# Performance work log

Hardware: AMD Instinct MI355X
Metric: run time of the kernel (lower is better)

## Reference

```python
import jax, jax.numpy as jnp
import numpy as np

N_CELL, N_WELL = 200000, 2000
E_CC, E_CW = 1200000, 200000
CF, WF, H = 16, 8, 128
NUM_PHASES, OUT_SEQ = 3, 25
OUT = NUM_PHASES * OUT_SEQ  # 75


def setup_inputs() -> dict:
    key = jax.random.key(0)
    ks = jax.random.split(key, 24)
    p = lambda k, shp: jax.random.normal(k, shp, dtype=jnp.float32) * 0.02
    return {
        "cell_x": jax.random.normal(ks[0], (N_CELL, CF), dtype=jnp.float32),
        "well_x": jax.random.normal(ks[1], (N_WELL, WF), dtype=jnp.float32),
        "edge_index_cell": jax.random.randint(ks[2], (2, E_CC), 0, N_CELL),
        "edge_well_src": jax.random.randint(ks[3], (E_CW,), 0, N_CELL),
        "edge_well_dst": jax.random.randint(ks[4], (E_CW,), 0, N_WELL),
        # input projections
        "W_cell": p(ks[5], (CF, H)), "b_cell": jnp.zeros((H,), jnp.float32),
        "W_well": p(ks[6], (WF, H)), "b_well": jnp.zeros((H,), jnp.float32),
        # SAGEConv cell->cell: lin_l (on aggregated neighbors, has bias), lin_r (on root, no bias)
        "Wl_cc": p(ks[7], (H, H)), "bl_cc": jnp.zeros((H,), jnp.float32),
        "Wr_cc": p(ks[8], (H, H)),
        # SAGEConv cell->well (bipartite)
        "Wl_cw": p(ks[9], (H, H)), "bl_cw": jnp.zeros((H,), jnp.float32),
        "Wr_cw": p(ks[10], (H, H)),
        # well MLP
        "W_m1": p(ks[11], (H, H)), "b_m1": jnp.zeros((H,), jnp.float32),
        "W_m2": p(ks[12], (H, OUT)), "b_m2": jnp.zeros((OUT,), jnp.float32),
    }


def _mean_aggr(msgs, dst, num_segments):
    # PyG 'mean' aggregation: sum per destination / neighbor count; 0 for isolated nodes.
    s = jax.ops.segment_sum(msgs, dst, num_segments=num_segments)
    c = jax.ops.segment_sum(jnp.ones((dst.shape[0], 1), msgs.dtype), dst, num_segments=num_segments)
    return s / jnp.maximum(c, 1.0)


def reference(cell_x, well_x, edge_index_cell, edge_well_src, edge_well_dst,
              W_cell, b_cell, W_well, b_well,
              Wl_cc, bl_cc, Wr_cc, Wl_cw, bl_cw, Wr_cw,
              W_m1, b_m1, W_m2, b_m2):
    cell_h = cell_x @ W_cell + b_cell                      # [N_cell, H]
    well_h = well_x @ W_well + b_well                      # [N_well, H]

    # SAGEConv(cell_h, edge_index_cell): gather source feats, mean-scatter to dst
    src, dst = edge_index_cell[0], edge_index_cell[1]
    agg_c = _mean_aggr(cell_h[src], dst, N_CELL)           # [N_cell, H]
    cell_h = agg_c @ Wl_cc + bl_cc + cell_h @ Wr_cc

    # Bipartite SAGEConv((cell_h, well_h), edge_well): aggregate cells into wells
    agg_w = _mean_aggr(cell_h[edge_well_src], edge_well_dst, N_WELL)  # [N_well, H]
    well_h = agg_w @ Wl_cw + bl_cw + well_h @ Wr_cw

    # well MLP head
    h = jax.nn.relu(well_h @ W_m1 + b_m1)
    out = h @ W_m2 + b_m2                                  # [N_well, 75]
    return out.reshape(-1, NUM_PHASES, OUT_SEQ)            # [N_well, 3, 25]
```

## Files before the change

### kernel.cpp

```cpp
#include <hip/hip_runtime.h>

#define N_CELL 200000
#define N_WELL 2000
#define E_CC   1200000
#define E_CW   200000
#define CF     16
#define WF     8
#define H      128
#define OUTF   75

#define CAP_C  16
#define CAP_W  224
#define OVF_CAP 16384
#define WPB    4

#define BLD_T  307200

__device__ __forceinline__ float b2f(unsigned short u) {
    union { unsigned int i; float f; } v; v.i = ((unsigned int)u) << 16; return v.f;
}
__device__ __forceinline__ unsigned short f2b(float f) {
    union { float f; unsigned int i; } v; v.f = f;
    unsigned int i = v.i;
    return (unsigned short)((i + 0x7fffu + ((i >> 16) & 1u)) >> 16);
}
__device__ __forceinline__ float lo16(unsigned int v) { return b2f((unsigned short)(v & 0xffffu)); }
__device__ __forceinline__ float hi16(unsigned int v) { return b2f((unsigned short)(v >> 16)); }
__device__ __forceinline__ float ldf(const void* p, int i, int bf) {
    return bf ? b2f(((const unsigned short*)p)[i]) : ((const float*)p)[i];
}

__device__ __forceinline__ int sniff128(const unsigned int* __restrict__ x)
{
    __shared__ int cnt[128];
    int t = threadIdx.x;
    unsigned a = x[t], b = x[t + 128];
    unsigned ea = (a >> 7) & 0xffu, eb = (b >> 7) & 0xffu;
    cnt[t] = ((ea >= 110u && ea <= 135u) ? 1 : 0) + ((eb >= 110u && eb <= 135u) ? 1 : 0);
    __syncthreads();
    for (int o = 64; o > 0; o >>= 1) { if (t < o) cnt[t] += cnt[t + o]; __syncthreads(); }
    int r = (cnt[0] >= 192) ? 1 : 0;
    __syncthreads();
    return r;
}

__global__ __launch_bounds__(128) void k_setup1(const unsigned int* __restrict__ x256,
                                                const void* __restrict__ W_cell,
                                                const void* __restrict__ b_cell,
                                                const void* __restrict__ Wl,
                                                const void* __restrict__ Wr,
                                                const void* __restrict__ bl,
                                                float* __restrict__ G1, float* __restrict__ G2,
                                                float* __restrict__ g1v, float* __restrict__ g2v,
                                                int* __restrict__ flag,
                                                unsigned int* __restrict__ zero_p, int zero_dw)
{
    int f = threadIdx.x, b = blockIdx.x;
    if (b < 16) {
        int bf = sniff128(x256);
        float s1 = 0.f, s2 = 0.f;
        for (int j = 0; j < H; ++j) {
            float wc = ldf(W_cell, b * H + j, bf);
            s1 += wc * ldf(Wl, j * H + f, bf);
            s2 += wc * ldf(Wr, j * H + f, bf);
        }
        G1[b * H + f] = s1; G2[b * H + f] = s2;
    } else if (b == 16) {
        int bf = sniff128(x256);
        float s1 = 0.f, s2 = 0.f;
        for (int j = 0; j < H; ++j) {
            float bc = ldf(b_cell, j, bf);
            s1 += bc * ldf(Wl, j * H + f, bf);
            s2 += bc * ldf(Wr, j * H + f, bf);
        }
        g1v[f] = s1; g2v[f] = s2 + ldf(bl, f, bf);
    } else if (b == 17) {
        int bf = sniff128(x256);
        if (f == 0) flag[0] = bf;
    } else {
        for (int i = (b - 18) * 128 + f; i < zero_dw; i += 64 * 128)
            zero_p[i] = 0u;
    }
}

__global__ __launch_bounds__(128) void k_setup2(const float* __restrict__ G1, const float* __restrict__ G2,
                                                const float* __restrict__ g1v, const float* __restrict__ g2v,
                                                const void* __restrict__ Wl_cw,
                                                const void* __restrict__ bl_cw,
                                                const void* __restrict__ Wr_cw,
                                                const void* __restrict__ W_well,
                                                const void* __restrict__ b_well,
                                                const void* __restrict__ Wm1, const void* __restrict__ Wm2,
                                                const void* __restrict__ bm1, const void* __restrict__ bm2,
                                                const int* __restrict__ flag,
                                                float* __restrict__ A1, float* __restrict__ A2,
                                                float* __restrict__ Bm,
                                                float* __restrict__ a1, float* __restrict__ a2,
                                                float* __restrict__ b0,
                                                float* __restrict__ Wm1f, float* __restrict__ Wm2f,
                                                float* __restrict__ bm1f, float* __restrict__ bm2f)
{
    int f = threadIdx.x, b = blockIdx.x, bf = flag[0];
    if (b < 16) {
        float s1 = 0.f, s2 = 0.f;
        for (int j = 0; j < H; ++j) {
            float wl = ldf(Wl_cw, j * H + f, bf);
            s1 += G1[b * H + j] * wl;
            s2 += G2[b * H + j] * wl;
        }
        A1[b * H + f] = s1; A2[b * H + f] = s2;
    } else if (b < 24) {
        int k = b - 16;
        float s = 0.f;
        for (int j = 0; j < H; ++j)
            s += ldf(W_well, k * H + j, bf) * ldf(Wr_cw, j * H + f, bf);
        Bm[k * H + f] = s;
    } else if (b == 24) {
        float s1 = 0.f, s2 = 0.f, s3 = 0.f;
        for (int j = 0; j < H; ++j) {
            float wl = ldf(Wl_cw, j * H + f, bf);
            s1 += g1v[j] * wl;
            s2 += g2v[j] * wl;
            s3 += ldf(b_well, j, bf) * ldf(Wr_cw, j * H + f, bf);
        }
        a1[f] = s1; a2[f] = s2; b0[f] = s3 + ldf(bl_cw, f, bf);
    } else {
        int i = (b - 25) * 128 + f;
        if (i < H * H) Wm1f[i] = ldf(Wm1, i, bf);
        else if (i < H * H + H * OUTF) Wm2f[i - H * H] = ldf(Wm2, i - H * H, bf);
        else if (i < H * H + H * OUTF + H) bm1f[i - H * H - H * OUTF] = ldf(bm1, i - H * H - H * OUTF, bf);
        else if (i < H * H + H * OUTF + H + OUTF) bm2f[i - H * H - H * OUTF - H] = ldf(bm2, i - H * H - H * OUTF - H, bf);
    }
}

__global__ void k_markw(const int* __restrict__ ews, const int* __restrict__ ewd,
                        unsigned char* __restrict__ mark,
                        int* __restrict__ counts_w, int* __restrict__ buckets_w)
{
    int i = blockIdx.x * 256 + threadIdx.x;
    if (i < E_CW) {
        unsigned c = (unsigned)ews[i];
        if (c < N_CELL) mark[c] = 1;
        unsigned d = (unsigned)ewd[i];
        if (d < N_WELL) {
            int s = atomicAdd(&counts_w[d], 1);
            if (s < CAP_W) buckets_w[d * CAP_W + s] = ews[i];
        }
    }
}

__global__ __launch_bounds__(256) void k_build(const int* __restrict__ cc_src, const int* __restrict__ cc_dst,
                                               const unsigned char* __restrict__ mark,
                                               int* __restrict__ counts_c,
                                               int* __restrict__ buckets_c,
                                               int* __restrict__ ovf_cnt, int2* __restrict__ ovf)
{
    int i = blockIdx.x * 256 + threadIdx.x;
    int e0 = i, e1 = i + BLD_T, e2 = i + 2 * BLD_T, e3 = i + 3 * BLD_T;
    unsigned d0 = (e0 < E_CC) ? (unsigned)cc_dst[e0] : 0xFFFFFFFFu;
    unsigned d1 = (e1 < E_CC) ? (unsigned)cc_dst[e1] : 0xFFFFFFFFu;
    unsigned d2 = (e2 < E_CC) ? (unsigned)cc_dst[e2] : 0xFFFFFFFFu;
    unsigned d3 = (e3 < E_CC) ? (unsigned)cc_dst[e3] : 0xFFFFFFFFu;
    bool m0 = (d0 < N_CELL) && mark[d0];
    bool m1 = (d1 < N_CELL) && mark[d1];
    bool m2 = (d2 < N_CELL) && mark[d2];
    bool m3 = (d3 < N_CELL) && mark[d3];
    int s0 = m0 ? cc_src[e0] : 0;
    int s1 = m1 ? cc_src[e1] : 0;
    int s2 = m2 ? cc_src[e2] : 0;
    int s3 = m3 ? cc_src[e3] : 0;
    if (m0) {
        int p = atomicAdd(&counts_c[d0], 1);
        if (p < CAP_C) buckets_c[d0 * CAP_C + p] = s0;
        else { int q = atomicAdd(ovf_cnt, 1); if (q < OVF_CAP) { ovf[q].x = (int)d0; ovf[q].y = s0; } }
    }
    if (m1) {
        int p = atomicAdd(&counts_c[d1], 1);
        if (p < CAP_C) buckets_c[d1 * CAP_C + p] = s1;
        else { int q = atomicAdd(ovf_cnt, 1); if (q < OVF_CAP) { ovf[q].x = (int)d1; ovf[q].y = s1; } }
    }
    if (m2) {
        int p = atomicAdd(&counts_c[d2], 1);
        if (p < CAP_C) buckets_c[d2 * CAP_C + p] = s2;
        else { int q = atomicAdd(ovf_cnt, 1); if (q < OVF_CAP) { ovf[q].x = (int)d2; ovf[q].y = s2; } }
    }
    if (m3) {
        int p = atomicAdd(&counts_c[d3], 1);
        if (p < CAP_C) buckets_c[d3 * CAP_C + p] = s3;
        else { int q = atomicAdd(ovf_cnt, 1); if (q < OVF_CAP) { ovf[q].x = (int)d3; ovf[q].y = s3; } }
    }
}

__global__ __launch_bounds__(256) void k_aggA(const void* __restrict__ xr,
                                              const int* __restrict__ flag,
                                              const unsigned char* __restrict__ mark,
                                              const int* __restrict__ counts_c,
                                              const int* __restrict__ buckets_c,
                                              float* __restrict__ y)
{
    int gid = (blockIdx.x * 256 + threadIdx.x) >> 3;
    int jl = threadIdx.x & 7;
    if (gid >= N_CELL) return;
    if (!mark[gid]) return;
    int bf = flag[0];
    int cnt = counts_c[gid]; if (cnt < 0) cnt = 0;
    int lim = (cnt < CAP_C) ? cnt : CAP_C;
    float acc[16];
#pragma unroll
    for (int k = 0; k < 16; ++k) acc[k] = 0.f;

    for (int j = jl; j < lim; j += 8) {
        unsigned s = (unsigned)buckets_c[gid * CAP_C + j]; if (s >= N_CELL) s = 0;
        if (bf) {
            uint4 a = ((const uint4*)xr)[(size_t)s * 2];
            uint4 b = ((const uint4*)xr)[(size_t)s * 2 + 1];
            acc[0] += lo16(a.x);  acc[1] += hi16(a.x);
            acc[2] += lo16(a.y);  acc[3] += hi16(a.y);
            acc[4] += lo16(a.z);  acc[5] += hi16(a.z);
            acc[6] += lo16(a.w);  acc[7] += hi16(a.w);
            acc[8] += lo16(b.x);  acc[9] += hi16(b.x);
            acc[10] += lo16(b.y); acc[11] += hi16(b.y);
            acc[12] += lo16(b.z); acc[13] += hi16(b.z);
            acc[14] += lo16(b.w); acc[15] += hi16(b.w);
        } else {
            const float4* p = (const float4*)xr + (size_t)s * 4;
#pragma unroll
            for (int q = 0; q < 4; ++q) {
                float4 v = p[q];
                acc[4 * q]     += v.x; acc[4 * q + 1] += v.y;
                acc[4 * q + 2] += v.z; acc[4 * q + 3] += v.w;
            }
        }
    }
#pragma unroll
    for (int m = 1; m < 8; m <<= 1) {
#pragma unroll
        for (int k = 0; k < 16; ++k) acc[k] += __shfl_xor(acc[k], m, 64);
    }
    float sc = (cnt > 0) ? (1.0f / (float)cnt) : 0.0f;
    float2 st; st.x = acc[2 * jl] * sc; st.y = acc[2 * jl + 1] * sc;
    ((float2*)y)[(size_t)gid * 8 + jl] = st;
}

__global__ __launch_bounds__(256) void k_ovf(const void* __restrict__ xr,
                                             const int* __restrict__ flag,
                                             const int* __restrict__ ovf_cnt,
                                             const int2* __restrict__ ovf,
                                             const int* __restrict__ counts_c,
                                             float* __restrict__ y)
{
    int gid = (blockIdx.x * 256 + threadIdx.x) >> 3;
    int jl = threadIdx.x & 7;
    int n = ovf_cnt[0]; if (n > OVF_CAP) n = OVF_CAP;
    if (gid >= n) return;
    int bf = flag[0];
    unsigned d = (unsigned)ovf[gid].x; if (d >= N_CELL) d = 0;
    unsigned s = (unsigned)ovf[gid].y; if (s >= N_CELL) s = 0;
    int cnt = counts_c[d];
    float inv = (cnt > 0) ? (1.0f / (float)cnt) : 0.0f;
    float v0, v1;
    if (bf) {
        unsigned int u = ((const unsigned int*)xr)[(size_t)s * 8 + jl];
        v0 = lo16(u); v1 = hi16(u);
    } else {
        v0 = ((const float*)xr)[(size_t)s * 16 + 2 * jl];
        v1 = ((const float*)xr)[(size_t)s * 16 + 2 * jl + 1];
    }
    atomicAdd(&y[(size_t)d * 16 + 2 * jl], v0 * inv);
    atomicAdd(&y[(size_t)d * 16 + 2 * jl + 1], v1 * inv);
}

__global__ __launch_bounds__(256) void k_wellagg(const void* __restrict__ xr,
                                                 const int* __restrict__ flag,
                                                 const float* __restrict__ y,
                                                 const int* __restrict__ counts_c,
                                                 const int* __restrict__ counts_w,
                                                 const int* __restrict__ buckets_w,
                                                 const void* __restrict__ wx,
                                                 const float* __restrict__ A1, const float* __restrict__ A2,
                                                 const float* __restrict__ Bm,
                                                 const float* __restrict__ a1, const float* __restrict__ a2,
                                                 const float* __restrict__ b0,
                                                 float* __restrict__ Z)
{
    __shared__ float sP[16], sR[16], sq[1];
    int w = blockIdx.x, t = threadIdx.x, bf = flag[0];
    int g = t >> 3, jl = t & 7;
    if (t < 16) { sP[t] = 0.f; sR[t] = 0.f; }
    if (t == 16) sq[0] = 0.f;
    __syncthreads();

    int cntw = counts_w[w]; if (cntw < 0) cntw = 0;
    int lim = (cntw < CAP_W) ? cntw : CAP_W;

    float p0 = 0.f, p1 = 0.f, r0 = 0.f, r1 = 0.f, qn = 0.f;
    const unsigned int* x32 = (const unsigned int*)xr;
    const float* xf = (const float*)xr;

    for (int e = g; e < lim; e += 32) {
        unsigned c = (unsigned)buckets_w[w * CAP_W + e]; if (c >= N_CELL) c = 0;
        float2 yv = ((const float2*)y)[(size_t)c * 8 + jl];
        p0 += yv.x; p1 += yv.y;
        if (bf) {
            unsigned int u = x32[(size_t)c * 8 + jl];
            r0 += lo16(u); r1 += hi16(u);
        } else {
            r0 += xf[(size_t)c * 16 + 2 * jl];
            r1 += xf[(size_t)c * 16 + 2 * jl + 1];
        }
        if (jl == 0) qn += (counts_c[c] > 0) ? 1.0f : 0.0f;
    }
    atomicAdd(&sP[2 * jl], p0);
    atomicAdd(&sP[2 * jl + 1], p1);
    atomicAdd(&sR[2 * jl], r0);
    atomicAdd(&sR[2 * jl + 1], r1);
    if (jl == 0 && qn != 0.f) atomicAdd(&sq[0], qn);
    __syncthreads();

    int f = t;
    if (f < H) {
        float inv = (cntw > 0) ? (1.0f / (float)cntw) : 0.0f;
        float mask = (cntw > 0) ? 1.0f : 0.0f;
        float wh = (sq[0] * inv) * a1[f] + a2[f];
#pragma unroll
        for (int k = 0; k < 16; ++k)
            wh += (sP[k] * inv) * A1[k * H + f] + (sR[k] * inv) * A2[k * H + f];
        wh *= mask;
        wh += b0[f];
#pragma unroll
        for (int k = 0; k < WF; ++k)
            wh += ldf(wx, w * WF + k, bf) * Bm[k * H + f];
        Z[(size_t)w * H + f] = wh;
    }
}

__global__ __launch_bounds__(128) void k_head(const float* __restrict__ Z,
                                              const float* __restrict__ Wm1f, const float* __restrict__ Wm2f,
                                              const float* __restrict__ bm1f, const float* __restrict__ bm2f,
                                              const int* __restrict__ flag,
                                              void* __restrict__ outp)
{
    __shared__ float sz[WPB][H], sh[WPB][H];
    int w0 = blockIdx.x * WPB, t = threadIdx.x, bf = flag[0];
    float4 zv = ((const float4*)(Z + (size_t)w0 * H))[t];
    ((float4*)&sz[0][0])[t] = zv;
    __syncthreads();

    float acc[WPB];
#pragma unroll
    for (int i = 0; i < WPB; ++i) acc[i] = bm1f[t];
    for (int k = 0; k < H; ++k) {
        float wm = Wm1f[k * H + t];
#pragma unroll
        for (int i = 0; i < WPB; ++i) acc[i] += sz[i][k] * wm;
    }
#pragma unroll
    for (int i = 0; i < WPB; ++i) sh[i][t] = fmaxf(acc[i], 0.f);
    __syncthreads();

    if (t < OUTF) {
        float o[WPB];
#pragma unroll
        for (int i = 0; i < WPB; ++i) o[i] = bm2f[t];
        for (int k = 0; k < H; ++k) {
            float wm = Wm2f[k * OUTF + t];
#pragma unroll
            for (int i = 0; i < WPB; ++i) o[i] += sh[i][k] * wm;
        }
        if (bf) {
#pragma unroll
            for (int i = 0; i < WPB; ++i)
                ((unsigned short*)outp)[(size_t)(w0 + i) * OUTF + t] = f2b(o[i]);
        } else {
#pragma unroll
            for (int i = 0; i < WPB; ++i)
                ((float*)outp)[(size_t)(w0 + i) * OUTF + t] = o[i];
        }
    }
}

extern "C" void kernel_launch(void* const* d_in, const int* in_sizes, int n_in,
                              void* d_out, int out_size, void* d_ws, size_t ws_size,
                              hipStream_t stream)
{
    const void* cell_x = d_in[0];
    const void* well_x = d_in[1];
    const int* eic = (const int*)d_in[2];
    const int* ews = (const int*)d_in[3];
    const int* ewd = (const int*)d_in[4];
    const void* W_cell = d_in[5];
    const void* b_cell = d_in[6];
    const void* W_well = d_in[7];
    const void* b_well = d_in[8];
    const void* Wl_cc = d_in[9];
    const void* bl_cc = d_in[10];
    const void* Wr_cc = d_in[11];
    const void* Wl_cw = d_in[12];
    const void* bl_cw = d_in[13];
    const void* Wr_cw = d_in[14];
    const void* W_m1 = d_in[15];
    const void* b_m1 = d_in[16];
    const void* W_m2 = d_in[17];
    const void* b_m2 = d_in[18];
    (void)in_sizes; (void)n_in; (void)out_size; (void)ws_size;

    const int* cc_src = eic;
    const int* cc_dst = eic + E_CC;

    char* wsp = (char*)d_ws;
    size_t off = 0;
    auto carve = [&](size_t bytes) -> char* {
        char* p = wsp + off;
        off = (off + bytes + 255) & ~(size_t)255;
        return p;
    };

    float* G1   = (float*)carve(16 * H * 4);
    float* G2   = (float*)carve(16 * H * 4);
    float* g1v  = (float*)carve(H * 4);
    float* g2v  = (float*)carve(H * 4);
    float* A1   = (float*)carve(16 * H * 4);
    float* A2   = (float*)carve(16 * H * 4);
    float* Bm   = (float*)carve(WF * H * 4);
    float* a1   = (float*)carve(H * 4);
    float* a2   = (float*)carve(H * 4);
    float* b0   = (float*)carve(H * 4);
    float* Wm1f = (float*)carve(H * H * 4);
    float* Wm2f = (float*)carve(H * OUTF * 4);
    float* bm1f = (float*)carve(H * 4);
    float* bm2f = (float*)carve(OUTF * 4);
    int*   flag = (int*)carve(256);
    size_t zero_beg = off;
    int*   counts   = (int*)carve((size_t)(N_CELL + N_WELL) * 4);
    int*   counts_c = counts;
    int*   counts_w = counts + N_CELL;
    unsigned char* mark = (unsigned char*)carve((size_t)N_CELL);
    int*   ovf_cnt  = (int*)carve(256);
    size_t zero_end = off;
    int*   buckets_c = (int*)carve((size_t)N_CELL * CAP_C * 4);
    int*   buckets_w = (int*)carve((size_t)N_WELL * CAP_W * 4);
    float* y         = (float*)carve((size_t)N_CELL * 16 * 4);
    int2*  ovf       = (int2*)carve((size_t)OVF_CAP * 8);
    float* Z         = (float*)carve((size_t)N_WELL * H * 4);

    int zero_dw = (int)((zero_end - zero_beg) / 4);

    k_setup1<<<82, 128, 0, stream>>>((const unsigned int*)cell_x, W_cell, b_cell, Wl_cc, Wr_cc, bl_cc,
                                     G1, G2, g1v, g2v, flag,
                                     (unsigned int*)((char*)d_ws + zero_beg), zero_dw);
    k_setup2<<<230, 128, 0, stream>>>(G1, G2, g1v, g2v, Wl_cw, bl_cw, Wr_cw, W_well, b_well,
                                      W_m1, W_m2, b_m1, b_m2, flag,
                                      A1, A2, Bm, a1, a2, b0, Wm1f, Wm2f, bm1f, bm2f);
    k_markw<<<(E_CW + 255) / 256, 256, 0, stream>>>(ews, ewd, mark, counts_w, buckets_w);
    k_build<<<BLD_T / 256, 256, 0, stream>>>(cc_src, cc_dst, mark, counts_c, buckets_c, ovf_cnt, ovf);
    k_aggA<<<(N_CELL * 8 + 255) / 256, 256, 0, stream>>>(cell_x, flag, mark, counts_c, buckets_c, y);
    k_ovf<<<(OVF_CAP * 8 + 255) / 256, 256, 0, stream>>>(cell_x, flag, ovf_cnt, ovf, counts_c, y);
    k_wellagg<<<N_WELL, 256, 0, stream>>>(cell_x, flag, y, counts_c, counts_w, buckets_w,
                                          well_x, A1, A2, Bm, a1, a2, b0, Z);
    k_head<<<N_WELL / WPB, 128, 0, stream>>>(Z, Wm1f, Wm2f, bm1f, bm2f, flag, d_out);
}
```

Measured before the change: 289.7 us.

## Partition bucket build by XCD so each die handles its own destination slice

Rewrites the edge bucketing kernel so each group of 8 consecutive blocks covers one 8000-edge chunk, and each block keeps only edges whose destination's (d>>5)&7 matches its blockIdx&7. The intent is that atomics and bucket writes for a given destination range stay within one XCD's L2, assuming round-robin block-to-XCD dispatch, which cuts cross-die coherence traffic. In exchange every edge's dst is read by 8 blocks, an 8x increase in dst index reads, though these mostly hit cache. The gain depends on the hardware's block scheduling order, which the code does not control.

```diff
diff --git a/kernel.cpp b/kernel.cpp
--- a/kernel.cpp
+++ b/kernel.cpp
@@ -14,7 +14,8 @@
 #define OVF_CAP 16384
 #define WPB    4
 
-#define BLD_T  307200
+#define NCHUNK 150
+#define BCHUNK 8000
 
 __device__ __forceinline__ float b2f(unsigned short u) {
     union { unsigned int i; float f; } v; v.i = ((unsigned int)u) << 16; return v.f;
@@ -155,39 +156,18 @@
                                                int* __restrict__ buckets_c,
                                                int* __restrict__ ovf_cnt, int2* __restrict__ ovf)
 {
-    int i = blockIdx.x * 256 + threadIdx.x;
-    int e0 = i, e1 = i + BLD_T, e2 = i + 2 * BLD_T, e3 = i + 3 * BLD_T;
-    unsigned d0 = (e0 < E_CC) ? (unsigned)cc_dst[e0] : 0xFFFFFFFFu;
-    unsigned d1 = (e1 < E_CC) ? (unsigned)cc_dst[e1] : 0xFFFFFFFFu;
-    unsigned d2 = (e2 < E_CC) ? (unsigned)cc_dst[e2] : 0xFFFFFFFFu;
-    unsigned d3 = (e3 < E_CC) ? (unsigned)cc_dst[e3] : 0xFFFFFFFFu;
-    bool m0 = (d0 < N_CELL) && mark[d0];
-    bool m1 = (d1 < N_CELL) && mark[d1];
-    bool m2 = (d2 < N_CELL) && mark[d2];
-    bool m3 = (d3 < N_CELL) && mark[d3];
-    int s0 = m0 ? cc_src[e0] : 0;
-    int s1 = m1 ? cc_src[e1] : 0;
-    int s2 = m2 ? cc_src[e2] : 0;
-    int s3 = m3 ? cc_src[e3] : 0;
-    if (m0) {
-        int p = atomicAdd(&counts_c[d0], 1);
-        if (p < CAP_C) buckets_c[d0 * CAP_C + p] = s0;
-        else { int q = atomicAdd(ovf_cnt, 1); if (q < OVF_CAP) { ovf[q].x = (int)d0; ovf[q].y = s0; } }
-    }
-    if (m1) {
-        int p = atomicAdd(&counts_c[d1], 1);
-        if (p < CAP_C) buckets_c[d1 * CAP_C + p] = s1;
-        else { int q = atomicAdd(ovf_cnt, 1); if (q < OVF_CAP) { ovf[q].x = (int)d1; ovf[q].y = s1; } }
-    }
-    if (m2) {
-        int p = atomicAdd(&counts_c[d2], 1);
-        if (p < CAP_C) buckets_c[d2 * CAP_C + p] = s2;
-        else { int q = atomicAdd(ovf_cnt, 1); if (q < OVF_CAP) { ovf[q].x = (int)d2; ovf[q].y = s2; } }
-    }
-    if (m3) {
-        int p = atomicAdd(&counts_c[d3], 1);
-        if (p < CAP_C) buckets_c[d3 * CAP_C + p] = s3;
-        else { int q = atomicAdd(ovf_cnt, 1); if (q < OVF_CAP) { ovf[q].x = (int)d3; ovf[q].y = s3; } }
+    int xcd = blockIdx.x & 7;
+    int cb  = blockIdx.x >> 3;
+    int beg = cb * BCHUNK, end = beg + BCHUNK;
+    if (end > E_CC) end = E_CC;
+    for (int e = beg + threadIdx.x; e < end; e += 256) {
+        unsigned d = (unsigned)cc_dst[e];
+        if (d < N_CELL && (int)((d >> 5) & 7u) == xcd && mark[d]) {
+            int s = cc_src[e];
+            int p = atomicAdd(&counts_c[d], 1);
+            if (p < CAP_C) buckets_c[d * CAP_C + p] = s;
+            else { int q = atomicAdd(ovf_cnt, 1); if (q < OVF_CAP) { ovf[q].x = (int)d; ovf[q].y = s; } }
+        }
     }
 }
 
@@ -452,7 +432,7 @@
                                       W_m1, W_m2, b_m1, b_m2, flag,
                                       A1, A2, Bm, a1, a2, b0, Wm1f, Wm2f, bm1f, bm2f);
     k_markw<<<(E_CW + 255) / 256, 256, 0, stream>>>(ews, ewd, mark, counts_w, buckets_w);
-    k_build<<<BLD_T / 256, 256, 0, stream>>>(cc_src, cc_dst, mark, counts_c, buckets_c, ovf_cnt, ovf);
+    k_build<<<8 * NCHUNK, 256, 0, stream>>>(cc_src, cc_dst, mark, counts_c, buckets_c, ovf_cnt, ovf);
     k_aggA<<<(N_CELL * 8 + 255) / 256, 256, 0, stream>>>(cell_x, flag, mark, counts_c, buckets_c, y);
     k_ovf<<<(OVF_CAP * 8 + 255) / 256, 256, 0, stream>>>(cell_x, flag, ovf_cnt, ovf, counts_c, y);
     k_wellagg<<<N_WELL, 256, 0, stream>>>(cell_x, flag, y, counts_c, counts_w, buckets_w,
```

Result: faster. 275.4 us, median of 2 (-4.9%).
